# Performance work log

Hardware: AMD Instinct MI355X
Metric: run time of the kernel (lower is better)

Reference implementation:

```python
import jax, jax.numpy as jnp
import numpy as np

G, N_PER_G, S, DEG, EMB, LAYERS = 64, 64, 8, 4, 128, 5


def _build_structure():
    """Ring graphs (degree DEG) with per-root windows of S nodes.
    Returns all integer index arrays for the tuple-sparse conv."""
    N = G * N_PER_G
    P = N * S          # (i, j) pairs
    T = P * S          # (i, j, k) tuples, k fastest
    deltas = np.array([1, 2, -1, -2])
    roots = np.arange(N)
    gbase = (roots // N_PER_G) * N_PER_G
    # window(i): S consecutive nodes in the same graph
    win = ((roots % N_PER_G)[:, None] + np.arange(S)) % N_PER_G + gbase[:, None]  # [N,S]
    tupleid0 = np.repeat(roots, S * S)
    tupleid1 = np.repeat(win.ravel(), S)
    # valid (k-offset, delta) combos so that l = k + delta stays inside window
    ok_g, di_g = np.meshgrid(np.arange(S), np.arange(DEG), indexing='ij')
    ol = ok_g + deltas[di_g]
    m = (ol >= 0) & (ol < S)
    ok_v, di_v, ol_v = ok_g[m], di_g[m], ol[m]        # [26]
    pairs = np.arange(P)
    msg_dst = (pairs[:, None] * S + ok_v[None, :]).ravel()
    msg_src = (pairs[:, None] * S + ol_v[None, :]).ravel()
    i_of_pair = pairs // S
    k_glob = ((i_of_pair % N_PER_G)[:, None] + ok_v[None, :]) % N_PER_G \
             + ((i_of_pair // N_PER_G) * N_PER_G)[:, None]
    msg_edge = (k_glob * DEG + di_v[None, :]).ravel()  # edge id = u*DEG + delta_idx
    seg_pair = np.arange(T) // S   # tuple -> (i,j) pair
    seg_node = np.arange(P) // S   # pair  -> root node i
    batch = np.repeat(np.arange(G), N_PER_G)
    return N, P, T, tupleid0, tupleid1, msg_src, msg_dst, msg_edge, seg_pair, seg_node, batch


def setup_inputs() -> dict:
    rng = np.random.default_rng(0)
    N, P, T, t0, t1, ms, md, me, sp, sn, batch = _build_structure()
    E = N * DEG
    i32 = lambda a: jnp.asarray(a, jnp.int32)
    key = jax.random.key(0)
    ks = jax.random.split(key, 8)
    sc = 0.05
    inp = {
        'x': i32(rng.integers(0, 32, N)),
        'edge_attr': i32(rng.integers(0, 16, E)),
        'tuplefeat': i32(rng.integers(0, 16, (T, 2))),
        'batch': i32(batch),
        'tupleid0': i32(t0), 'tupleid1': i32(t1),
        'msg_src': i32(ms), 'msg_dst': i32(md), 'msg_edge': i32(me),
        'seg_pair': i32(sp), 'seg_node': i32(sn),
        'num_graphs': G,
        'emb_x': jax.random.normal(ks[0], (32, EMB), jnp.float32) * sc,
        'emb_ea': jax.random.normal(ks[1], (16, EMB), jnp.float32) * sc,
        'emb_tf': jax.random.normal(ks[2], (16, EMB // 2), jnp.float32) * sc,
        'w_ti': jax.random.normal(ks[3], (EMB, EMB), jnp.float32) * sc,
        'b_ti': jnp.zeros((EMB,), jnp.float32),
        'w_conv': jax.random.normal(ks[4], (LAYERS, EMB, EMB), jnp.float32) * sc,
        'b_conv': jnp.zeros((LAYERS, EMB), jnp.float32),
        'w_pred': jax.random.normal(ks[5], (EMB, 1), jnp.float32) * sc,
        'b_pred': jnp.zeros((1,), jnp.float32),
    }
    return inp


def reference(x, edge_attr, tuplefeat, batch, tupleid0, tupleid1,
              msg_src, msg_dst, msg_edge, seg_pair, seg_node, num_graphs,
              emb_x, emb_ea, emb_tf, w_ti, b_ti, w_conv, b_conv, w_pred, b_pred):
    T = tuplefeat.shape[0]
    N = x.shape[0]
    P = seg_node.shape[0]
    # InputEncoder
    xe = emb_x[x]                                   # [N, E]
    ea = emb_ea[edge_attr]                          # [E_edges, E]
    tf = emb_tf[tuplefeat].reshape(T, -1)           # [T, 2, E/2] -> [T, E]
    # tupleinit: x[t0] * lin(x)[t1] * tuplefeat
    Xv = xe[tupleid0] * (xe @ w_ti + b_ti)[tupleid1] * tf   # [T, E]

    def layer(carry, wb):
        w, b = wb
        msgs = carry[msg_src] * ea[msg_edge]                         # [M, E]
        agg = jax.ops.segment_sum(msgs, msg_dst, num_segments=T)      # [T, E]
        return carry + jax.nn.relu(agg @ w + b), None                 # residual

    Xv, _ = jax.lax.scan(layer, Xv, (w_conv, b_conv))
    # pooling2tuple (max over k), pooling2nodes (sum over j), npool (sum over batch)
    pair = jax.ops.segment_max(Xv, seg_pair, num_segments=P)          # [P, E]
    node = jax.ops.segment_sum(pair, seg_node, num_segments=N)        # [N, E]
    graph = jax.ops.segment_sum(node, batch, num_segments=num_graphs) # [G, E]
    return graph @ w_pred + b_pred                                    # [G, 1]
```

## Files before the change

kernel.cpp:

```cpp
#include <hip/hip_runtime.h>
#include <hip/hip_bf16.h>

#define EMB 128

typedef __attribute__((ext_vector_type(8))) short short8;
typedef __attribute__((ext_vector_type(4))) float floatx4;
typedef __attribute__((ext_vector_type(2))) float v2f;

static constexpr int OKv[26] = {0,0,1,1,1,2,2,2,2,3,3,3,3,4,4,4,4,5,5,5,5,6,6,6,7,7};
static constexpr int DIv[26] = {0,1,0,1,2,0,1,2,3,0,1,2,3,0,1,2,3,0,1,2,3,0,2,3,2,3};
static constexpr int OLv[26] = {1,2,2,3,0,3,4,1,0,4,5,2,1,5,6,3,2,6,7,4,3,7,5,4,6,5};

__device__ __forceinline__ v2f ldv2(const float* p) { return *(const v2f*)p; }

__device__ __forceinline__ unsigned bf16_rne_hi(float x) {
  unsigned u = __float_as_uint(x);
  return (u + 0x7FFFu + ((u >> 16) & 1u)) & 0xFFFF0000u;
}
__device__ __forceinline__ float bf16hi_f(float x) {
  return __uint_as_float(bf16_rne_hi(x));
}
__device__ __forceinline__ unsigned cvt_pk_bf16(float a, float b) {
  __hip_bfloat162 h = __float22bfloat162_rn(make_float2(a, b));
  unsigned r; __builtin_memcpy(&r, &h, 4); return r;
}

union FragU { unsigned u[4]; uint4 q; short8 v; };


__global__ __launch_bounds__(512) void prep_kernel(
    const float* __restrict__ emb_x,
    const float* __restrict__ w_ti,
    const float* __restrict__ b_ti,
    const float* __restrict__ w_conv,
    const float* __restrict__ b_pred,
    float* __restrict__ lin32,
    uint4* __restrict__ wfrag,
    float* __restrict__ out) {
  const int b = blockIdx.x, tid = threadIdx.x;
  if (b < 32) {
    __shared__ float red[4][EMB];
    const int e = tid & 127, fh = tid >> 7;
    const float* xr = emb_x + b * EMB;
    float s = 0.f;
    #pragma unroll 8
    for (int f = fh * 32; f < fh * 32 + 32; ++f)
      s = fmaf(xr[f], w_ti[f * EMB + e], s);
    red[fh][e] = s;
    __syncthreads();
    if (fh == 0)
      lin32[b * EMB + e] =
          b_ti[e] + ((red[0][e] + red[1][e]) + (red[2][e] + red[3][e]));
  } else if (b < 72) {
    const int id   = (b - 32) * 512 + tid;
    const int lane = id & 63;
    const int f    = id >> 6;
    const int pass = f & 1;
    const int u    = (f >> 1) & 7;
    const int t    = (f >> 4) & 3;
    const int l    = f >> 6;
    const int q    = lane >> 4, n = lane & 15;
    const int cN   = 2 * ((u >> 1) * 16 + n) + (u & 1);
    unsigned w[4] = {0u, 0u, 0u, 0u};
    #pragma unroll
    for (int j = 0; j < 8; ++j) {
      const int kk = t * 32 + q * 8 + j;
      float val = w_conv[l * (EMB * EMB) + kk * EMB + cN];
      if (pass) val = val - bf16hi_f(val);
      const unsigned bb = bf16_rne_hi(val);
      w[j >> 1] |= (j & 1) ? bb : (bb >> 16);
    }
    wfrag[id] = make_uint4(w[0], w[1], w[2], w[3]);
  } else {
    if (tid < 64) out[tid] = b_pred[0];
  }
}

__global__ __launch_bounds__(256)
void i2gnn_mfma(
    const int* __restrict__ x,
    const int* __restrict__ edge_attr,
    const int* __restrict__ tuplefeat,
    const float* __restrict__ emb_x,
    const float* __restrict__ emb_tf,
    const float* __restrict__ emb_ea,
    const float* __restrict__ lin32,
    const float* __restrict__ b_conv,
    const float* __restrict__ w_pred,
    const uint4* __restrict__ wfrag,
    float* __restrict__ out)
{
  __shared__ __align__(16) unsigned fragA[2 * 64 * 68];

  const int tid = threadIdx.x;
  const int wv = tid >> 6, lane = tid & 63;
  const int m16 = lane & 15, q2 = lane >> 4;
  const int pc = wv * 16 + m16;
  const int c0 = pc * 2;

  const int i = blockIdx.x;
  const int ibase = i & ~63, io = i & 63;
  const int g = i >> 6;

  unsigned pk[4] = {0u, 0u, 0u, 0u};
  #pragma unroll
  for (int m = 0; m < 26; ++m) {
    const int kg = ibase + ((io + OKv[m]) & 63);
    const unsigned a = (unsigned)edge_attr[(kg << 2) + DIv[m]];
    pk[m >> 3] |= a << ((m & 7) * 4);
  }

  const int xi = x[i];
  const v2f xe = ldv2(emb_x + xi * EMB + c0);
  v2f lj[2];
  #pragma unroll
  for (int ps = 0; ps < 2; ++ps) {
    const int jn = ibase + ((io + 2 * q2 + ps) & 63);
    lj[ps] = ldv2(lin32 + x[jn] * EMB + c0);
  }
  v2f X2[4][4];
  #pragma unroll
  for (int mt = 0; mt < 4; ++mt) {
    const int ps = mt & 1, kb = (mt >> 1) * 4;
    const int t0 = (i * 8 + 2 * q2 + ps) << 3;
    const v2f xl = xe * lj[ps];
    #pragma unroll
    for (int r = 0; r < 4; ++r) {
      const int2 tf2 = *(const int2*)(tuplefeat + 2 * (t0 + kb + r));
      const int row = (c0 < 64) ? tf2.x : tf2.y;
      const v2f tf = ldv2(emb_tf + row * 64 + (c0 & 63));
      X2[mt][r] = xl * tf;
    }
  }

  for (int l = 0; l < 5; ++l) {
    v2f acc[2][8];
    #pragma unroll
    for (int ps = 0; ps < 2; ++ps)
      #pragma unroll
      for (int k = 0; k < 8; ++k) acc[ps][k] = (v2f){0.f, 0.f};
    #pragma unroll
    for (int m = 0; m < 26; ++m) {
      const unsigned attr = (pk[m >> 3] >> ((m & 7) * 4)) & 15u;
      const v2f e = ldv2(emb_ea + attr * EMB + c0);
      const int ok = OKv[m], ol = OLv[m];
      const int mtb = 2 * (ol >> 2), rl = ol & 3;
      acc[0][ok] += X2[mtb + 0][rl] * e;
      acc[1][ok] += X2[mtb + 1][rl] * e;
    }
    #pragma unroll
    for (int ps = 0; ps < 2; ++ps)
      #pragma unroll
      for (int k = 0; k < 8; ++k) {
        const v2f a = acc[ps][k];
        const unsigned hi = cvt_pk_bf16(a.x, a.y);
        v2f hf; hf.x = __uint_as_float(hi << 16);
                hf.y = __uint_as_float(hi & 0xFFFF0000u);
        const v2f r = a - hf;
        const int row = (ps + 2 * (k >> 2)) * 16 + q2 * 4 + (k & 3);
        fragA[row * 68 + pc] = hi;
        fragA[4352 + row * 68 + pc] = cvt_pk_bf16(r.x, r.y);
      }
    __syncthreads();

    floatx4 C[2][4];
    #pragma unroll
    for (int v = 0; v < 2; ++v)
      #pragma unroll
      for (int mt = 0; mt < 4; ++mt) C[v][mt] = (floatx4){0.f, 0.f, 0.f, 0.f};

    #pragma unroll
    for (int kt = 0; kt < 4; ++kt) {
      const uint4* wp0 = wfrag + ((((l * 4 + kt) * 8 + 2 * wv) * 2) << 6);
      FragU B0h, B0l, B1h, B1l;
      B0h.q = wp0[lane];        B0l.q = wp0[64 + lane];
      B1h.q = wp0[128 + lane];  B1l.q = wp0[192 + lane];
      #pragma unroll
      for (int mt = 0; mt < 4; ++mt) {
        const unsigned* fa = fragA + (mt * 16 + m16) * 68 + kt * 16 + q2 * 4;
        FragU Ah, Al;
        Ah.q = *(const uint4*)fa;
        Al.q = *(const uint4*)(fa + 4352);
        C[0][mt] = __builtin_amdgcn_mfma_f32_16x16x32_bf16(Ah.v, B0h.v, C[0][mt], 0, 0, 0);
        C[0][mt] = __builtin_amdgcn_mfma_f32_16x16x32_bf16(Al.v, B0h.v, C[0][mt], 0, 0, 0);
        C[0][mt] = __builtin_amdgcn_mfma_f32_16x16x32_bf16(Ah.v, B0l.v, C[0][mt], 0, 0, 0);
        C[1][mt] = __builtin_amdgcn_mfma_f32_16x16x32_bf16(Ah.v, B1h.v, C[1][mt], 0, 0, 0);
        C[1][mt] = __builtin_amdgcn_mfma_f32_16x16x32_bf16(Al.v, B1h.v, C[1][mt], 0, 0, 0);
        C[1][mt] = __builtin_amdgcn_mfma_f32_16x16x32_bf16(Ah.v, B1l.v, C[1][mt], 0, 0, 0);
      }
    }
    __syncthreads();

    const v2f bc = ldv2(b_conv + l * EMB + c0);
    #pragma unroll
    for (int mt = 0; mt < 4; ++mt)
      #pragma unroll
      for (int r = 0; r < 4; ++r) {
        v2f o; o.x = C[0][mt][r]; o.y = C[1][mt][r];
        o += bc;
        o.x = fmaxf(o.x, 0.f); o.y = fmaxf(o.y, 0.f);
        X2[mt][r] += o;
      }
  }

  const v2f wp = ldv2(w_pred + c0);
  v2f p0 = (v2f){-3.4e38f, -3.4e38f}, p1 = p0;
  #pragma unroll
  for (int r = 0; r < 4; ++r) {
    p0.x = fmaxf(p0.x, fmaxf(X2[0][r].x, X2[2][r].x));
    p0.y = fmaxf(p0.y, fmaxf(X2[0][r].y, X2[2][r].y));
    p1.x = fmaxf(p1.x, fmaxf(X2[1][r].x, X2[3][r].x));
    p1.y = fmaxf(p1.y, fmaxf(X2[1][r].y, X2[3][r].y));
  }
  const v2f ps = (p0 + p1) * wp;
  float s = ps.x + ps.y;
  #pragma unroll
  for (int off = 32; off; off >>= 1) s += __shfl_xor(s, off, 64);
  if (lane == 0) atomicAdd(out + g, s);
}

extern "C" void kernel_launch(void* const* d_in, const int* in_sizes, int n_in,
                              void* d_out, int out_size, void* d_ws, size_t ws_size,
                              hipStream_t stream) {
  const int*   x         = (const int*)d_in[0];
  const int*   edge_attr = (const int*)d_in[1];
  const int*   tuplefeat = (const int*)d_in[2];
  const float* emb_x     = (const float*)d_in[12];
  const float* emb_ea    = (const float*)d_in[13];
  const float* emb_tf    = (const float*)d_in[14];
  const float* w_ti      = (const float*)d_in[15];
  const float* b_ti      = (const float*)d_in[16];
  const float* w_conv    = (const float*)d_in[17];
  const float* b_conv    = (const float*)d_in[18];
  const float* w_pred    = (const float*)d_in[19];
  const float* b_pred    = (const float*)d_in[20];
  float* out = (float*)d_out;
  float* lin32 = (float*)d_ws;
  uint4* wfrag = (uint4*)((char*)d_ws + 32 * EMB * 4);

  hipLaunchKernelGGL(prep_kernel, dim3(73), dim3(512), 0, stream,
                     emb_x, w_ti, b_ti, w_conv, b_pred, lin32, wfrag, out);
  hipLaunchKernelGGL(i2gnn_mfma, dim3(4096), dim3(256), 0, stream,
                     x, edge_attr, tuplefeat, emb_x, emb_tf, emb_ea, lin32,
                     b_conv, w_pred, wfrag, out);
}
```

Before: 299.6 us.

## Process two roots per block and overlap message VALU with MFMA

```diff
diff --git a/kernel.cpp b/kernel.cpp
--- a/kernel.cpp
+++ b/kernel.cpp
@@ -98,56 +98,73 @@
   const int pc = wv * 16 + m16;
   const int c0 = pc * 2;
 
-  const int i = blockIdx.x;
-  const int ibase = i & ~63, io = i & 63;
-  const int g = i >> 6;
-
-  unsigned pk[4] = {0u, 0u, 0u, 0u};
-  #pragma unroll
-  for (int m = 0; m < 26; ++m) {
-    const int kg = ibase + ((io + OKv[m]) & 63);
-    const unsigned a = (unsigned)edge_attr[(kg << 2) + DIv[m]];
-    pk[m >> 3] |= a << ((m & 7) * 4);
-  }
-
-  const int xi = x[i];
-  const v2f xe = ldv2(emb_x + xi * EMB + c0);
-  v2f lj[2];
-  #pragma unroll
-  for (int ps = 0; ps < 2; ++ps) {
-    const int jn = ibase + ((io + 2 * q2 + ps) & 63);
-    lj[ps] = ldv2(lin32 + x[jn] * EMB + c0);
-  }
-  v2f X2[4][4];
-  #pragma unroll
-  for (int mt = 0; mt < 4; ++mt) {
-    const int ps = mt & 1, kb = (mt >> 1) * 4;
-    const int t0 = (i * 8 + 2 * q2 + ps) << 3;
-    const v2f xl = xe * lj[ps];
-    #pragma unroll
-    for (int r = 0; r < 4; ++r) {
-      const int2 tf2 = *(const int2*)(tuplefeat + 2 * (t0 + kb + r));
-      const int row = (c0 < 64) ? tf2.x : tf2.y;
-      const v2f tf = ldv2(emb_tf + row * 64 + (c0 & 63));
-      X2[mt][r] = xl * tf;
-    }
-  }
-
-  for (int l = 0; l < 5; ++l) {
-    v2f acc[2][8];
+  const int i0 = blockIdx.x * 2;
+  const int g  = i0 >> 6;
+
+  int pkk[2][4];
+  v2f xe[2];
+  v2f lj[2][2];
+  int tbase[2];
+  #pragma unroll
+  for (int r = 0; r < 2; ++r) {
+    const int i = i0 + r;
+    const int ibase = i & ~63, io = i & 63;
+    unsigned p0 = 0, p1 = 0, p2 = 0, p3 = 0;
+    #pragma unroll
+    for (int m = 0; m < 26; ++m) {
+      const int kg = ibase + ((io + OKv[m]) & 63);
+      const unsigned a = (unsigned)edge_attr[(kg << 2) + DIv[m]];
+      const unsigned sh = (m & 7) * 4;
+      if ((m >> 3) == 0) p0 |= a << sh;
+      else if ((m >> 3) == 1) p1 |= a << sh;
+      else if ((m >> 3) == 2) p2 |= a << sh;
+      else p3 |= a << sh;
+    }
+    pkk[r][0] = __builtin_amdgcn_readfirstlane(p0);
+    pkk[r][1] = __builtin_amdgcn_readfirstlane(p1);
+    pkk[r][2] = __builtin_amdgcn_readfirstlane(p2);
+    pkk[r][3] = __builtin_amdgcn_readfirstlane(p3);
+    xe[r] = ldv2(emb_x + x[i] * EMB + c0);
+    #pragma unroll
+    for (int ps = 0; ps < 2; ++ps) {
+      const int jn = ibase + ((io + 2 * q2 + ps) & 63);
+      lj[r][ps] = ldv2(lin32 + x[jn] * EMB + c0);
+    }
+    tbase[r] = i * 64;
+  }
+
+  v2f X[2][4][4];
+  #pragma unroll
+  for (int r = 0; r < 2; ++r)
+    #pragma unroll
+    for (int mt = 0; mt < 4; ++mt) {
+      const int ps = mt & 1, kb = (mt >> 1) * 4;
+      const int t0 = tbase[r] + (2 * q2 + ps) * 8;
+      const v2f xl = xe[r] * lj[r][ps];
+      #pragma unroll
+      for (int rr = 0; rr < 4; ++rr) {
+        const int2 tf2 = *(const int2*)(tuplefeat + 2 * (t0 + kb + rr));
+        const int row = (c0 < 64) ? tf2.x : tf2.y;
+        X[r][mt][rr] = xl * ldv2(emb_tf + row * 64 + (c0 & 63));
+      }
+    }
+
+  auto msg = [&](int r, v2f acc[2][8]) {
     #pragma unroll
     for (int ps = 0; ps < 2; ++ps)
       #pragma unroll
       for (int k = 0; k < 8; ++k) acc[ps][k] = (v2f){0.f, 0.f};
     #pragma unroll
     for (int m = 0; m < 26; ++m) {
-      const unsigned attr = (pk[m >> 3] >> ((m & 7) * 4)) & 15u;
+      const unsigned attr = ((unsigned)pkk[r][m >> 3] >> ((m & 7) * 4)) & 15u;
       const v2f e = ldv2(emb_ea + attr * EMB + c0);
       const int ok = OKv[m], ol = OLv[m];
       const int mtb = 2 * (ol >> 2), rl = ol & 3;
-      acc[0][ok] += X2[mtb + 0][rl] * e;
-      acc[1][ok] += X2[mtb + 1][rl] * e;
-    }
+      acc[0][ok] += X[r][mtb + 0][rl] * e;
+      acc[1][ok] += X[r][mtb + 1][rl] * e;
+    }
+  };
+  auto pack = [&](v2f acc[2][8]) {
     #pragma unroll
     for (int ps = 0; ps < 2; ++ps)
       #pragma unroll
@@ -156,19 +173,17 @@
         const unsigned hi = cvt_pk_bf16(a.x, a.y);
         v2f hf; hf.x = __uint_as_float(hi << 16);
                 hf.y = __uint_as_float(hi & 0xFFFF0000u);
-        const v2f r = a - hf;
+        const v2f rr = a - hf;
         const int row = (ps + 2 * (k >> 2)) * 16 + q2 * 4 + (k & 3);
         fragA[row * 68 + pc] = hi;
-        fragA[4352 + row * 68 + pc] = cvt_pk_bf16(r.x, r.y);
-      }
-    __syncthreads();
-
-    floatx4 C[2][4];
+        fragA[4352 + row * 68 + pc] = cvt_pk_bf16(rr.x, rr.y);
+      }
+  };
+  auto mfma = [&](int l, floatx4 C[2][4]) {
     #pragma unroll
     for (int v = 0; v < 2; ++v)
       #pragma unroll
       for (int mt = 0; mt < 4; ++mt) C[v][mt] = (floatx4){0.f, 0.f, 0.f, 0.f};
-
     #pragma unroll
     for (int kt = 0; kt < 4; ++kt) {
       const uint4* wp0 = wfrag + ((((l * 4 + kt) * 8 + 2 * wv) * 2) << 6);
@@ -189,31 +204,59 @@
         C[1][mt] = __builtin_amdgcn_mfma_f32_16x16x32_bf16(Ah.v, B1l.v, C[1][mt], 0, 0, 0);
       }
     }
-    __syncthreads();
-
+  };
+  auto residual = [&](int r, int l, floatx4 C[2][4]) {
     const v2f bc = ldv2(b_conv + l * EMB + c0);
     #pragma unroll
     for (int mt = 0; mt < 4; ++mt)
       #pragma unroll
-      for (int r = 0; r < 4; ++r) {
-        v2f o; o.x = C[0][mt][r]; o.y = C[1][mt][r];
+      for (int rr = 0; rr < 4; ++rr) {
+        v2f o; o.x = C[0][mt][rr]; o.y = C[1][mt][rr];
         o += bc;
         o.x = fmaxf(o.x, 0.f); o.y = fmaxf(o.y, 0.f);
-        X2[mt][r] += o;
-      }
+        X[r][mt][rr] += o;
+      }
+  };
+
+  v2f accA[2][8], accB[2][8];
+  floatx4 C[2][4];
+
+  msg(0, accA);
+  pack(accA);
+  __syncthreads();
+  #pragma unroll 1
+  for (int l = 0; l < 5; ++l) {
+    mfma(l, C);
+    msg(1, accB);
+    residual(0, l, C);
+    __syncthreads();
+    pack(accB);
+    __syncthreads();
+    mfma(l, C);
+    if (l < 4) msg(0, accA);
+    residual(1, l, C);
+    __syncthreads();
+    if (l < 4) {
+      pack(accA);
+      __syncthreads();
+    }
   }
 
   const v2f wp = ldv2(w_pred + c0);
-  v2f p0 = (v2f){-3.4e38f, -3.4e38f}, p1 = p0;
-  #pragma unroll
-  for (int r = 0; r < 4; ++r) {
-    p0.x = fmaxf(p0.x, fmaxf(X2[0][r].x, X2[2][r].x));
-    p0.y = fmaxf(p0.y, fmaxf(X2[0][r].y, X2[2][r].y));
-    p1.x = fmaxf(p1.x, fmaxf(X2[1][r].x, X2[3][r].x));
-    p1.y = fmaxf(p1.y, fmaxf(X2[1][r].y, X2[3][r].y));
-  }
-  const v2f ps = (p0 + p1) * wp;
-  float s = ps.x + ps.y;
+  float s = 0.f;
+  #pragma unroll
+  for (int r = 0; r < 2; ++r) {
+    v2f p0 = (v2f){-3.4e38f, -3.4e38f}, p1 = p0;
+    #pragma unroll
+    for (int rr = 0; rr < 4; ++rr) {
+      p0.x = fmaxf(p0.x, fmaxf(X[r][0][rr].x, X[r][2][rr].x));
+      p0.y = fmaxf(p0.y, fmaxf(X[r][0][rr].y, X[r][2][rr].y));
+      p1.x = fmaxf(p1.x, fmaxf(X[r][1][rr].x, X[r][3][rr].x));
+      p1.y = fmaxf(p1.y, fmaxf(X[r][1][rr].y, X[r][3][rr].y));
+    }
+    const v2f pr = (p0 + p1) * wp;
+    s += pr.x + pr.y;
+  }
   #pragma unroll
   for (int off = 32; off; off >>= 1) s += __shfl_xor(s, off, 64);
   if (lane == 0) atomicAdd(out + g, s);
@@ -240,7 +283,7 @@
 
   hipLaunchKernelGGL(prep_kernel, dim3(73), dim3(512), 0, stream,
                      emb_x, w_ti, b_ti, w_conv, b_pred, lin32, wfrag, out);
-  hipLaunchKernelGGL(i2gnn_mfma, dim3(4096), dim3(256), 0, stream,
+  hipLaunchKernelGGL(i2gnn_mfma, dim3(2048), dim3(256), 0, stream,
                      x, edge_attr, tuplefeat, emb_x, emb_tf, emb_ea, lin32,
                      b_conv, w_pred, wfrag, out);
 }
```

Result: slower. 379.8 us (+26.8%).
